# Kernel tuning notes

Measured on AMD Instinct MI355X. Metric: run time of the kernel, lower is better.

The kernel has to match this reference:

```python
import jax, jax.numpy as jnp
import numpy as np

L, D, H, F = 2, 512, 8, 2048
B, S = 1, 2048
DH = D // H
EPS = 1e-6
NEG = -1e9


def setup_inputs() -> dict:
    key = jax.random.key(0)
    ks = jax.random.split(key, 8)
    s = 0.02
    return {
        "x": jax.random.normal(ks[0], (B, S, D), jnp.float32),
        "enc_output": jax.random.normal(ks[1], (B, S, D), jnp.float32),
        # per-layer stacked params; axis 1 of attn weights = [wq, wk, wv, wo]
        "attn1_w": jax.random.normal(ks[2], (L, 4, D, D), jnp.float32) * s,
        "attn1_b": jnp.zeros((L, 4, D), jnp.float32),
        "attn2_w": jax.random.normal(ks[3], (L, 4, D, D), jnp.float32) * s,
        "attn2_b": jnp.zeros((L, 4, D), jnp.float32),
        "ffn_w1": jax.random.normal(ks[4], (L, D, F), jnp.float32) * s,
        "ffn_b1": jnp.zeros((L, F), jnp.float32),
        "ffn_w2": jax.random.normal(ks[5], (L, F, D), jnp.float32) * s,
        "ffn_b2": jnp.zeros((L, D), jnp.float32),
        # axis 1 = [norm1, norm2, norm3]
        "ln_g": jnp.ones((L, 3, D), jnp.float32),
        "ln_b": jnp.zeros((L, 3, D), jnp.float32),
    }


def positional_encoding(seq_len, num_feat):
    pos = jnp.arange(seq_len, dtype=jnp.float32)[:, None]
    dims = jnp.arange(num_feat, dtype=jnp.float32)[None, :]
    rates = 1.0 / jnp.power(10000.0, 2.0 * jnp.floor(dims / 2.0) / num_feat)
    ang = pos * rates  # [S, D]
    # keras module concatenates sines(even cols) and cosines(odd cols)
    return jnp.concatenate([jnp.sin(ang[:, 0::2]), jnp.cos(ang[:, 1::2])], axis=-1)[None]


def layer_norm(x, g, b):
    mu = jnp.mean(x, axis=-1, keepdims=True)
    var = jnp.mean(jnp.square(x - mu), axis=-1, keepdims=True)
    return (x - mu) * jax.lax.rsqrt(var + EPS) * g + b


def split_heads(x):
    b, s, _ = x.shape
    return x.reshape(b, s, H, DH).transpose(0, 2, 1, 3)  # [B,H,S,dh]


def mha(q_in, k_in, v_in, w, bias, mask):
    q = split_heads(q_in @ w[0] + bias[0])
    k = split_heads(k_in @ w[1] + bias[1])
    v = split_heads(v_in @ w[2] + bias[2])
    logits = jnp.einsum("bhqd,bhkd->bhqk", q, k) / jnp.sqrt(jnp.float32(DH))
    if mask is not None:
        logits = logits + mask * NEG
    weights = jax.nn.softmax(logits, axis=-1)
    out = jnp.einsum("bhqk,bhkd->bhqd", weights, v)
    b, _, s, _ = out.shape
    out = out.transpose(0, 2, 1, 3).reshape(b, s, D)
    return out @ w[3] + bias[3]


def decoder_forward(x, enc_output, attn1_w, attn1_b, attn2_w, attn2_b,
                    ffn_w1, ffn_b1, ffn_w2, ffn_b2, ln_g, ln_b):
    s = x.shape[1]
    x = x + positional_encoding(s, x.shape[2])
    causal = jnp.triu(jnp.ones((s, s), jnp.float32), k=1)[None, None]  # 1 = masked

    def layer(x, p):
        a1w, a1b, a2w, a2b, w1, b1, w2, b2, g, bn = p
        attn1 = mha(x, x, x, a1w, a1b, causal)
        x = layer_norm(x + attn1, g[0], bn[0])
        attn2 = mha(x, enc_output, enc_output, a2w, a2b, None)
        x = layer_norm(x + attn2, g[1], bn[1])
        ffn = jax.nn.relu(x @ w1 + b1) @ w2 + b2
        x = layer_norm(x + ffn, g[2], bn[2])
        return x, None

    x, _ = jax.lax.scan(layer, x, (attn1_w, attn1_b, attn2_w, attn2_b,
                                   ffn_w1, ffn_b1, ffn_w2, ffn_b2, ln_g, ln_b))
    return x


def reference(x, enc_output, attn1_w, attn1_b, attn2_w, attn2_b,
              ffn_w1, ffn_b1, ffn_w2, ffn_b2, ln_g, ln_b):
    return decoder_forward(x, enc_output, attn1_w, attn1_b, attn2_w, attn2_b,
                           ffn_w1, ffn_b1, ffn_w2, ffn_b2, ln_g, ln_b)
```

## Files before the change

kernel.cpp:

```cpp
#include <hip/hip_runtime.h>
#include <hip/hip_bf16.h>
#include <math.h>

#define S 2048
#define D 512
#define H 8
#define DH 64
#define F 2048
#define NLAYER 2

typedef __attribute__((ext_vector_type(8))) short bf16x8;
typedef __attribute__((ext_vector_type(4))) float f32x4;
typedef __hip_bfloat16 bf16;

typedef __attribute__((address_space(3))) unsigned int lds_u32;
typedef __attribute__((address_space(1))) const unsigned int glb_u32;

__device__ __forceinline__ void gld16(const void* g, void* l) {
    __builtin_amdgcn_global_load_lds((glb_u32*)g, (lds_u32*)l, 16, 0, 0);
}

__global__ void prep_kernel(const float* __restrict__ x, const float* __restrict__ enc,
                            float* __restrict__ xbF, bf16* __restrict__ xbB,
                            bf16* __restrict__ encB) {
    int idx = blockIdx.x * blockDim.x + threadIdx.x;
    if (idx >= S * D) return;
    int s = idx / D;
    int j = idx % D;
    int jj = (j < D / 2) ? j : j - D / 2;
    float rate = expf(-(float)jj * (logf(10000.0f) / (float)(D / 2)));
    float ang = (float)s * rate;
    float pe = (j < D / 2) ? sinf(ang) : cosf(ang);
    float v = x[idx] + pe;
    xbF[idx] = v;
    xbB[idx] = __float2bfloat16(v);
    encB[idx] = __float2bfloat16(enc[idx]);
}

__global__ __launch_bounds__(256)
void transpose_cvt_b(const float* __restrict__ in, bf16* __restrict__ out, int R, int C,
                     size_t inStride, size_t outL, size_t outM, int mpl)
{
    __shared__ float t[64][65];
    const int z = blockIdx.z;
    const float* src = in + (size_t)z * inStride;
    bf16* dst = out + (size_t)(z / mpl) * outL + (size_t)(z % mpl) * outM;
    const int rb = blockIdx.x * 64, cb = blockIdx.y * 64;
    for (int i = threadIdx.x; i < 4096; i += 256) {
        int r = i >> 6, c = i & 63;
        t[r][c] = src[(size_t)(rb + r) * C + cb + c];
    }
    __syncthreads();
    for (int i = threadIdx.x; i < 4096; i += 256) {
        int r = i >> 6, c = i & 63;
        dst[(size_t)(cb + r) * R + rb + c] = __float2bfloat16(t[c][r]);
    }
}

template<int BM, int BN, int BK, int MODE>
__global__ __launch_bounds__(256)
void gemm_bf16(const bf16* __restrict__ A, const bf16* __restrict__ Bt,
               const float* __restrict__ bias, float* __restrict__ outF,
               bf16* __restrict__ outB, int K, int ldc, int relu,
               bf16* __restrict__ q16, bf16* __restrict__ kh,
               bf16* __restrict__ vt, int qn, int kn)
{
    constexpr int MI = BM / 32, NJ = BN / 32;
    constexpr int SL = BK / 8;
    constexpr int KS = BK / 32;
    constexpr int HALF = (BM + BN) * BK * 2;
    constexpr int IA = BM * SL / 256, IB = BN * SL / 256;
    constexpr int TS = BN + 8;
    constexpr int LDS_VB = (MODE == 1) ? BM * TS * 2 : 0;
    constexpr int LDSZ = (2 * HALF > LDS_VB) ? 2 * HALF : LDS_VB;
    __shared__ char lds[LDSZ];
    const int tid = threadIdx.x;
    const int w = tid >> 6, l = tid & 63;
    const int l15 = l & 15, l4 = l >> 4;
    const int bm = blockIdx.y * BM, bn = blockIdx.x * BN;
    const int wr = (w >> 1) * (BM / 2), wc = (w & 1) * (BN / 2);

    f32x4 acc[MI][NJ] = {};

#define XV(row) ((BK == 64) ? ((row) & 7) : (((row) >> 1) & 3))
#define GSTAGE(k0, b)                                                          \
    {                                                                          \
        _Pragma("unroll")                                                      \
        for (int i = 0; i < IA; ++i) {                                         \
            int n = (w * IA + i) * 64 + l;                                     \
            int row = n / SL;                                                  \
            int sl = (n % SL) ^ XV(row);                                       \
            gld16(A + (size_t)(bm + row) * K + (k0) + sl * 8,                  \
                  lds + (b) * HALF + (w * IA + i) * 1024);                     \
        }                                                                      \
        _Pragma("unroll")                                                      \
        for (int i = 0; i < IB; ++i) {                                         \
            int n = (w * IB + i) * 64 + l;                                     \
            int row = n / SL;                                                  \
            int sl = (n % SL) ^ XV(row);                                       \
            gld16(Bt + (size_t)(bn + row) * K + (k0) + sl * 8,                 \
                  lds + (b) * HALF + BM * BK * 2 + (w * IB + i) * 1024);       \
        }                                                                      \
    }

    GSTAGE(0, 0);
    __syncthreads();
    int cur = 0;
    for (int k0 = 0; k0 < K; k0 += BK) {
        if (k0 + BK < K) GSTAGE(k0 + BK, cur ^ 1);
        const char* base = lds + cur * HALF;
        bf16x8 af[MI][KS], bfr[NJ][KS];
#pragma unroll
        for (int i = 0; i < MI; ++i) {
            int row = wr + i * 16 + l15;
#pragma unroll
            for (int s = 0; s < KS; ++s)
                af[i][s] = *(const bf16x8*)(base + row * (BK * 2)
                                            + (((s * 4 + l4) ^ XV(row)) << 4));
        }
#pragma unroll
        for (int j = 0; j < NJ; ++j) {
            int row = wc + j * 16 + l15;
#pragma unroll
            for (int s = 0; s < KS; ++s)
                bfr[j][s] = *(const bf16x8*)(base + BM * BK * 2 + row * (BK * 2)
                                             + (((s * 4 + l4) ^ XV(row)) << 4));
        }
#pragma unroll
        for (int s = 0; s < KS; ++s)
#pragma unroll
            for (int i = 0; i < MI; ++i)
#pragma unroll
                for (int j = 0; j < NJ; ++j)
                    acc[i][j] = __builtin_amdgcn_mfma_f32_16x16x32_bf16(af[i][s], bfr[j][s], acc[i][j], 0, 0, 0);
        __syncthreads();
        cur ^= 1;
    }
#undef GSTAGE
#undef XV

    if (MODE == 0) {
#pragma unroll
        for (int i = 0; i < MI; ++i)
#pragma unroll
            for (int j = 0; j < NJ; ++j)
#pragma unroll
                for (int q = 0; q < 4; ++q) {
                    int row = bm + wr + i * 16 + l4 * 4 + q;
                    int col = bn + wc + j * 16 + l15;
                    float v = acc[i][j][q] + bias[col];
                    if (relu) v = fmaxf(v, 0.f);
                    if (outF) outF[(size_t)row * ldc + col] = v;
                    if (outB) outB[(size_t)row * ldc + col] = __float2bfloat16(v);
                }
    } else {
        const int creg = (bn < qn) ? 0 : (bn < qn + kn ? 1 : 2);
        if (creg < 2) {
#pragma unroll
            for (int i = 0; i < MI; ++i)
#pragma unroll
                for (int j = 0; j < NJ; ++j)
#pragma unroll
                    for (int q = 0; q < 4; ++q) {
                        int row = bm + wr + i * 16 + l4 * 4 + q;
                        int col = bn + wc + j * 16 + l15;
                        float v = acc[i][j][q] + bias[col];
                        if (creg == 0) {
                            q16[(size_t)row * 512 + col] = __float2bfloat16(v);
                        } else {
                            int c2 = col - qn;
                            kh[((size_t)(c2 >> 6) * S + row) * 64 + (c2 & 63)] = __float2bfloat16(v);
                        }
                    }
        } else {
            short* t = (short*)lds;
#pragma unroll
            for (int i = 0; i < MI; ++i)
#pragma unroll
                for (int j = 0; j < NJ; ++j)
#pragma unroll
                    for (int q = 0; q < 4; ++q) {
                        int r = wr + i * 16 + l4 * 4 + q;
                        int c = wc + j * 16 + l15;
                        float v = acc[i][j][q] + bias[bn + c];
                        t[r * TS + c] = __builtin_bit_cast(short, __float2bfloat16(v));
                    }
            __syncthreads();
            const int dgb = bn - qn - kn;
            constexpr int SGR = BM / 8;
            for (int i2 = tid; i2 < BN * SGR; i2 += 256) {
                int dl = i2 / SGR;
                int s8 = (i2 % SGR) * 8;
                bf16x8 v;
#pragma unroll
                for (int jj = 0; jj < 8; ++jj)
                    v[jj] = t[(s8 + jj) * TS + dl];
                *(bf16x8*)(vt + (size_t)(dgb + dl) * S + bm + s8) = v;
            }
        }
    }
}

template<int CAUSAL>
__global__ __launch_bounds__(512)
void attn_mfma7(const bf16* __restrict__ Q, const bf16* __restrict__ Kh,
                const bf16* __restrict__ Vt, bf16* __restrict__ O)
{
    __shared__ char lds[82944];
    const int tid = threadIdx.x;
    const int w = tid >> 6, l = tid & 63;
    const int l15 = l & 15, l4 = l >> 4;
    const int g = w >> 2, wl = w & 3;
    const int h = blockIdx.x, qb = blockIdx.y;
    const int qw = qb * 64 + wl * 16;
    const int qr = qw + l15;
    char* plds = lds + 65536 + w * 2048;

    const float QSC = 0.1803368801f;
    bf16x8 aq[2];
#pragma unroll
    for (int s = 0; s < 2; ++s) {
        bf16x8 raw = *(const bf16x8*)(Q + (size_t)(qw + l15) * 512 + h * DH + s * 32 + l4 * 8);
#pragma unroll
        for (int j = 0; j < 8; ++j) {
            float f = __builtin_bit_cast(float, ((unsigned int)(unsigned short)raw[j]) << 16) * QSC;
            raw[j] = __builtin_bit_cast(short, __float2bfloat16(f));
        }
        aq[s] = raw;
    }

    f32x4 o[4] = {};
    float mrun = -1e30f, lrun = 0.f;
    const int cmax = CAUSAL ? qb : (S / 64 - 1);
    const int nits = cmax / 2 + 1;

#define STAGE(ii, p)                                                                \
    {                                                                               \
        const int cc = 2 * (ii) + g;                                                \
        if (cc <= cmax) {                                                           \
            const int kb2 = cc * 64;                                                \
            _Pragma("unroll")                                                       \
            for (int i = 0; i < 2; ++i) {                                           \
                int n = wl * 128 + i * 64 + l;                                      \
                int row = n >> 3;                                                   \
                int sl = (n & 7) ^ (row & 7);                                       \
                gld16(Kh + ((size_t)h * S + kb2 + row) * 64 + sl * 8,               \
                      lds + (p) * 32768 + g * 16384 + wl * 2048 + i * 1024);        \
                gld16(Vt + ((size_t)(h * 64 + row)) * S + kb2 + sl * 8,             \
                      lds + (p) * 32768 + g * 16384 + 8192 + wl * 2048 + i * 1024); \
            }                                                                       \
        }                                                                           \
    }

    STAGE(0, 0);
    __syncthreads();

    int cur = 0;
    for (int it = 0; it < nits; ++it) {
        if (it + 1 < nits) STAGE(it + 1, cur ^ 1);
        const int c = 2 * it + g;
        if (c <= cmax) {
            const char* kb = lds + cur * 32768 + g * 16384;
            const char* vb = kb + 8192;
            const int kbase = c * 64;

            f32x4 st[4];
            __builtin_amdgcn_s_setprio(1);
#pragma unroll
            for (int t = 0; t < 4; ++t) {
                f32x4 sacc = {0.f, 0.f, 0.f, 0.f};
#pragma unroll
                for (int s = 0; s < 2; ++s) {
                    bf16x8 kf = *(const bf16x8*)(kb + (t * 16 + l15) * 128
                                                 + (((s * 4 + l4) ^ (l15 & 7)) << 4));
                    sacc = __builtin_amdgcn_mfma_f32_16x16x32_bf16(kf, aq[s], sacc, 0, 0, 0);
                }
                st[t] = sacc;
            }
            __builtin_amdgcn_s_setprio(0);

            float mx = -1e30f;
#pragma unroll
            for (int t = 0; t < 4; ++t)
#pragma unroll
                for (int r = 0; r < 4; ++r) {
                    float v = st[t][r];
                    if (CAUSAL && c == cmax) {
                        int key = kbase + t * 16 + l4 * 4 + r;
                        if (key > qr) v = -1e30f;
                    }
                    st[t][r] = v;
                    mx = fmaxf(mx, v);
                }
            mx = fmaxf(mx, __shfl_xor(mx, 16));
            mx = fmaxf(mx, __shfl_xor(mx, 32));

            if (__any(mx > mrun + 8.0f)) {
                float mnew = fmaxf(mrun, mx);
                float scl = exp2f(mrun - mnew);
                mrun = mnew;
                lrun *= scl;
#pragma unroll
                for (int j = 0; j < 4; ++j) {
                    float sj = __shfl(scl, (l & 48) | (l4 * 4 + j));
#pragma unroll
                    for (int dt = 0; dt < 4; ++dt) o[dt][j] *= sj;
                }
            }

            float ps = 0.f;
#pragma unroll
            for (int t = 0; t < 4; ++t) {
                float e0 = exp2f(st[t][0] - mrun);
                float e1 = exp2f(st[t][1] - mrun);
                float e2 = exp2f(st[t][2] - mrun);
                float e3 = exp2f(st[t][3] - mrun);
                ps += (e0 + e1) + (e2 + e3);
                unsigned int lo = (unsigned int)(unsigned short)__builtin_bit_cast(short, __float2bfloat16(e0))
                                | ((unsigned int)(unsigned short)__builtin_bit_cast(short, __float2bfloat16(e1)) << 16);
                unsigned int hi = (unsigned int)(unsigned short)__builtin_bit_cast(short, __float2bfloat16(e2))
                                | ((unsigned int)(unsigned short)__builtin_bit_cast(short, __float2bfloat16(e3)) << 16);
                uint2 pk; pk.x = lo; pk.y = hi;
                int byte = (l15 * 128 + t * 32 + l4 * 8) ^ ((l15 & 7) << 4);
                *(uint2*)(plds + byte) = pk;
            }
            ps += __shfl_xor(ps, 16);
            ps += __shfl_xor(ps, 32);
            lrun += ps;

            bf16x8 pf[2];
#pragma unroll
            for (int s = 0; s < 2; ++s) {
                int byte = (l15 * 128 + s * 64 + l4 * 16) ^ ((l15 & 7) << 4);
                pf[s] = *(const bf16x8*)(plds + byte);
            }
            __builtin_amdgcn_s_setprio(1);
#pragma unroll
            for (int dt = 0; dt < 4; ++dt)
#pragma unroll
                for (int s = 0; s < 2; ++s) {
                    bf16x8 vf = *(const bf16x8*)(vb + (dt * 16 + l15) * 128
                                                 + (((s * 4 + l4) ^ (l15 & 7)) << 4));
                    o[dt] = __builtin_amdgcn_mfma_f32_16x16x32_bf16(pf[s], vf, o[dt], 0, 0, 0);
                }
            __builtin_amdgcn_s_setprio(0);
        }
        __syncthreads();
        cur ^= 1;
    }
#undef STAGE

#pragma unroll
    for (int dt = 0; dt < 4; ++dt)
#pragma unroll
        for (int j = 0; j < 4; ++j) {
            int q = l4 * 4 + j;
            int d = dt * 16 + l15;
            int byte = q * 128 + ((d * 2) ^ ((q & 7) << 4));
            *(short*)(plds + byte) = __builtin_bit_cast(short, __float2bfloat16(o[dt][j]));
        }
    if (l < 16) {
        *(float*)(lds + 81920 + w * 128 + l * 8) = mrun;
        *(float*)(lds + 81920 + w * 128 + l * 8 + 4) = lrun;
    }
    __syncthreads();

    {
        const int qt16 = tid >> 7;
        const int idx = tid & 127;
        const int q = idx >> 3;
        const int d0 = (idx & 7) * 8;
        const char* p0 = lds + 65536 + qt16 * 2048;
        const char* p1 = lds + 65536 + (qt16 + 4) * 2048;
        float m0 = *(const float*)(lds + 81920 + qt16 * 128 + q * 8);
        float l0 = *(const float*)(lds + 81920 + qt16 * 128 + q * 8 + 4);
        float m1 = *(const float*)(lds + 81920 + (qt16 + 4) * 128 + q * 8);
        float l1 = *(const float*)(lds + 81920 + (qt16 + 4) * 128 + q * 8 + 4);
        float mt = fmaxf(m0, m1);
        float f0 = exp2f(m0 - mt), f1 = exp2f(m1 - mt);
        float lt = f0 * l0 + f1 * l1;
        float inv = 1.f / lt;
        int byte = q * 128 + ((d0 * 2) ^ ((q & 7) << 4));
        bf16x8 a = *(const bf16x8*)(p0 + byte);
        bf16x8 b = *(const bf16x8*)(p1 + byte);
        bf16x8 r;
#pragma unroll
        for (int jj = 0; jj < 8; ++jj) {
            float va = __builtin_bit_cast(float, ((unsigned int)(unsigned short)a[jj]) << 16);
            float vb2 = __builtin_bit_cast(float, ((unsigned int)(unsigned short)b[jj]) << 16);
            r[jj] = __builtin_bit_cast(short, __float2bfloat16((f0 * va + f1 * vb2) * inv));
        }
        *(bf16x8*)(O + (size_t)(qb * 64 + qt16 * 16 + q) * D + h * DH + d0) = r;
    }
}

__global__ __launch_bounds__(128)
void add_ln_kernel(const float* __restrict__ a, const float* __restrict__ b,
                   const float* __restrict__ g, const float* __restrict__ beta,
                   float* __restrict__ outF, bf16* __restrict__ outB)
{
    const int row = blockIdx.x;
    const int tid = threadIdx.x;
    float4 av = *(const float4*)&a[(size_t)row * D + tid * 4];
    float4 bv = *(const float4*)&b[(size_t)row * D + tid * 4];
    float4 s;
    s.x = av.x + bv.x; s.y = av.y + bv.y; s.z = av.z + bv.z; s.w = av.w + bv.w;
    float sum = s.x + s.y + s.z + s.w;
    float sq = s.x * s.x + s.y * s.y + s.z * s.z + s.w * s.w;
#pragma unroll
    for (int off = 32; off > 0; off >>= 1) {
        sum += __shfl_xor(sum, off);
        sq  += __shfl_xor(sq, off);
    }
    __shared__ float red[4];
    if ((tid & 63) == 0) { red[(tid >> 6) * 2] = sum; red[(tid >> 6) * 2 + 1] = sq; }
    __syncthreads();
    sum = red[0] + red[2];
    sq  = red[1] + red[3];
    float mu = sum / (float)D;
    float var = sq / (float)D - mu * mu;
    float rs = rsqrtf(var + 1e-6f);
    float4 gv = *(const float4*)&g[tid * 4];
    float4 bt = *(const float4*)&beta[tid * 4];
    float4 o;
    o.x = (s.x - mu) * rs * gv.x + bt.x;
    o.y = (s.y - mu) * rs * gv.y + bt.y;
    o.z = (s.z - mu) * rs * gv.z + bt.z;
    o.w = (s.w - mu) * rs * gv.w + bt.w;
    *(float4*)&outF[(size_t)row * D + tid * 4] = o;
    if (outB) {
        outB[(size_t)row * D + tid * 4 + 0] = __float2bfloat16(o.x);
        outB[(size_t)row * D + tid * 4 + 1] = __float2bfloat16(o.y);
        outB[(size_t)row * D + tid * 4 + 2] = __float2bfloat16(o.z);
        outB[(size_t)row * D + tid * 4 + 3] = __float2bfloat16(o.w);
    }
}

extern "C" void kernel_launch(void* const* d_in, const int* in_sizes, int n_in,
                              void* d_out, int out_size, void* d_ws, size_t ws_size,
                              hipStream_t stream)
{
    const float* x   = (const float*)d_in[0];
    const float* enc = (const float*)d_in[1];
    const float* a1w = (const float*)d_in[2];
    const float* a1b = (const float*)d_in[3];
    const float* a2w = (const float*)d_in[4];
    const float* a2b = (const float*)d_in[5];
    const float* fw1 = (const float*)d_in[6];
    const float* fb1 = (const float*)d_in[7];
    const float* fw2 = (const float*)d_in[8];
    const float* fb2 = (const float*)d_in[9];
    const float* lng = (const float*)d_in[10];
    const float* lnb = (const float*)d_in[11];
    float* out = (float*)d_out;

    char* wsb = (char*)d_ws;
    float* xb   = (float*)(wsb);
    float* ao   = (float*)(wsb + ((size_t)4 << 20));
    bf16* xb16  = (bf16*)(wsb + ((size_t)8 << 20));
    bf16* enc16 = (bf16*)(wsb + ((size_t)10 << 20));
    bf16* att16 = (bf16*)(wsb + ((size_t)12 << 20));
    bf16* q16   = (bf16*)(wsb + ((size_t)14 << 20));
    bf16* kh16  = (bf16*)(wsb + ((size_t)16 << 20));
    bf16* vt16  = (bf16*)(wsb + ((size_t)18 << 20));
    bf16* ffh16 = att16;
    bf16* wts   = (bf16*)(wsb + ((size_t)20 << 20));
    const size_t WCH = 1048576;
    const size_t DD = (size_t)D * D, DF = (size_t)D * F;

    transpose_cvt_b<<<dim3(8, 8, 8), 256, 0, stream>>>(a1w, wts,            D, D, DD, WCH, DD, 4);
    transpose_cvt_b<<<dim3(8, 8, 8), 256, 0, stream>>>(a2w, wts + 2 * WCH,  D, D, DD, WCH, DD, 4);
    transpose_cvt_b<<<dim3(8, 32, 2), 256, 0, stream>>>(fw1, wts + 4 * WCH, D, F, DF, WCH, 0, 1);
    transpose_cvt_b<<<dim3(32, 8, 2), 256, 0, stream>>>(fw2, wts + 6 * WCH, F, D, DF, WCH, 0, 1);
    prep_kernel<<<(S * D + 255) / 256, 256, 0, stream>>>(x, enc, xb, xb16, enc16);

    for (int l = 0; l < NLAYER; ++l) {
        const bf16* A1T = wts + (size_t)(0 + l) * WCH;
        const bf16* A2T = wts + (size_t)(2 + l) * WCH;
        const bf16* W1T = wts + (size_t)(4 + l) * WCH;
        const bf16* W2T = wts + (size_t)(6 + l) * WCH;
        const float* b1v = a1b + (size_t)l * 4 * D;
        const float* b2v = a2b + (size_t)l * 4 * D;

        gemm_bf16<64, 64, 64, 1><<<dim3(24, 32), 256, 0, stream>>>(
            xb16, A1T, b1v, nullptr, nullptr, D, 0, 0, q16, kh16, vt16, 512, 512);
        attn_mfma7<1><<<dim3(H, S / 64), 512, 0, stream>>>(q16, kh16, vt16, att16);
        gemm_bf16<32, 64, 64, 0><<<dim3(8, 64), 256, 0, stream>>>(
            att16, A1T + 3 * DD, b1v + 3 * D, ao, nullptr, D, D, 0, nullptr, nullptr, nullptr, 0, 0);
        add_ln_kernel<<<S, 128, 0, stream>>>(xb, ao, lng + (size_t)(l * 3 + 0) * D, lnb + (size_t)(l * 3 + 0) * D, xb, xb16);

        gemm_bf16<32, 64, 64, 0><<<dim3(8, 64), 256, 0, stream>>>(
            xb16, A2T, b2v, nullptr, q16, D, 512, 0, nullptr, nullptr, nullptr, 0, 0);
        gemm_bf16<64, 64, 64, 1><<<dim3(16, 32), 256, 0, stream>>>(
            enc16, A2T + DD, b2v + D, nullptr, nullptr, D, 0, 0, q16, kh16, vt16, 0, 512);
        attn_mfma7<0><<<dim3(H, S / 64), 512, 0, stream>>>(q16, kh16, vt16, att16);
        gemm_bf16<32, 64, 64, 0><<<dim3(8, 64), 256, 0, stream>>>(
            att16, A2T + 3 * DD, b2v + 3 * D, ao, nullptr, D, D, 0, nullptr, nullptr, nullptr, 0, 0);
        add_ln_kernel<<<S, 128, 0, stream>>>(xb, ao, lng + (size_t)(l * 3 + 1) * D, lnb + (size_t)(l * 3 + 1) * D, xb, xb16);

        gemm_bf16<64, 64, 64, 0><<<dim3(32, 32), 256, 0, stream>>>(
            xb16, W1T, fb1 + (size_t)l * F, nullptr, ffh16, D, F, 1, nullptr, nullptr, nullptr, 0, 0);
        gemm_bf16<32, 64, 64, 0><<<dim3(8, 64), 256, 0, stream>>>(
            ffh16, W2T, fb2 + (size_t)l * D, ao, nullptr, F, D, 0, nullptr, nullptr, nullptr, 0, 0);
        float* dstF = (l == NLAYER - 1) ? out : xb;
        bf16* dstB = (l == NLAYER - 1) ? nullptr : xb16;
        add_ln_kernel<<<S, 128, 0, stream>>>(xb, ao, lng + (size_t)(l * 3 + 2) * D, lnb + (size_t)(l * 3 + 2) * D, dstF, dstB);
    }
}
```

Measured before the change: 289.6 us.

## Process two key chunks per wave group per stage in attention kernel

Each wave group now handles two 64-key chunks per iteration, with separate running max, sum and accumulator states that are merged at the end. The pipeline stage grows to 128 keys per group, so LDS use rises to about 145 KB and there are half as many barrier-separated iterations. Doubling in-flight MFMA work per wave is meant to give more instruction-level parallelism and cut synchronization overhead. The cost is more registers and LDS, which lowers occupancy, and the causal kernel gets coarser load balance at short rows.

```diff
diff --git a/kernel.cpp b/kernel.cpp
--- a/kernel.cpp
+++ b/kernel.cpp
@@ -203,10 +203,10 @@
 
 template<int CAUSAL>
 __global__ __launch_bounds__(512)
-void attn_mfma7(const bf16* __restrict__ Q, const bf16* __restrict__ Kh,
+void attn_mfma8(const bf16* __restrict__ Q, const bf16* __restrict__ Kh,
                 const bf16* __restrict__ Vt, bf16* __restrict__ O)
 {
-    __shared__ char lds[82944];
+    __shared__ char lds[148480];
     const int tid = threadIdx.x;
     const int w = tid >> 6, l = tid & 63;
     const int l15 = l & 15, l4 = l >> 4;
@@ -214,7 +214,7 @@
     const int h = blockIdx.x, qb = blockIdx.y;
     const int qw = qb * 64 + wl * 16;
     const int qr = qw + l15;
-    char* plds = lds + 65536 + w * 2048;
+    char* plds = lds + 131072 + w * 2048;
 
     const float QSC = 0.1803368801f;
     bf16x8 aq[2];
@@ -229,25 +229,27 @@
         aq[s] = raw;
     }
 
-    f32x4 o[4] = {};
-    float mrun = -1e30f, lrun = 0.f;
+    f32x4 oA[4] = {}, oB[4] = {};
+    float mA = -1e30f, lA = 0.f, mB = -1e30f, lB = 0.f;
     const int cmax = CAUSAL ? qb : (S / 64 - 1);
-    const int nits = cmax / 2 + 1;
+    const int nits = cmax / 4 + 1;
 
 #define STAGE(ii, p)                                                                \
     {                                                                               \
-        const int cc = 2 * (ii) + g;                                                \
-        if (cc <= cmax) {                                                           \
-            const int kb2 = cc * 64;                                                \
+        const int c0s = 4 * (ii) + 2 * g;                                           \
+        if (c0s <= cmax) {                                                          \
+            const int kb2 = c0s * 64;                                               \
             _Pragma("unroll")                                                       \
-            for (int i = 0; i < 2; ++i) {                                           \
-                int n = wl * 128 + i * 64 + l;                                      \
-                int row = n >> 3;                                                   \
-                int sl = (n & 7) ^ (row & 7);                                       \
-                gld16(Kh + ((size_t)h * S + kb2 + row) * 64 + sl * 8,               \
-                      lds + (p) * 32768 + g * 16384 + wl * 2048 + i * 1024);        \
-                gld16(Vt + ((size_t)(h * 64 + row)) * S + kb2 + sl * 8,             \
-                      lds + (p) * 32768 + g * 16384 + 8192 + wl * 2048 + i * 1024); \
+            for (int i = 0; i < 4; ++i) {                                           \
+                int n = wl * 256 + i * 64 + l;                                      \
+                int rowk = n >> 3;                                                  \
+                int slk = (n & 7) ^ (rowk & 7);                                     \
+                gld16(Kh + ((size_t)h * S + kb2 + rowk) * 64 + slk * 8,             \
+                      lds + (p) * 65536 + g * 32768 + wl * 4096 + i * 1024);        \
+                int rowv = n >> 4;                                                  \
+                int slv = (n & 15) ^ (rowv & 7);                                    \
+                gld16(Vt + ((size_t)(h * 64 + rowv)) * S + kb2 + slv * 8,           \
+                      lds + (p) * 65536 + g * 32768 + 16384 + wl * 4096 + i * 1024);\
             }                                                                       \
         }                                                                           \
     }
@@ -258,14 +260,15 @@
     int cur = 0;
     for (int it = 0; it < nits; ++it) {
         if (it + 1 < nits) STAGE(it + 1, cur ^ 1);
-        const int c = 2 * it + g;
-        if (c <= cmax) {
-            const char* kb = lds + cur * 32768 + g * 16384;
-            const char* vb = kb + 8192;
-            const int kbase = c * 64;
-
-            f32x4 st[4];
-            __builtin_amdgcn_s_setprio(1);
+        const int c0 = 4 * it + 2 * g;
+        const char* kb = lds + cur * 65536 + g * 32768;
+        const char* vb = kb + 16384;
+        const int actA = (c0 <= cmax);
+        const int actB = (c0 + 1 <= cmax);
+
+        f32x4 stA[4], stB[4];
+        __builtin_amdgcn_s_setprio(1);
+        if (actA) {
 #pragma unroll
             for (int t = 0; t < 4; ++t) {
                 f32x4 sacc = {0.f, 0.f, 0.f, 0.f};
@@ -275,80 +278,108 @@
                                                  + (((s * 4 + l4) ^ (l15 & 7)) << 4));
                     sacc = __builtin_amdgcn_mfma_f32_16x16x32_bf16(kf, aq[s], sacc, 0, 0, 0);
                 }
-                st[t] = sacc;
+                stA[t] = sacc;
             }
-            __builtin_amdgcn_s_setprio(0);
-
-            float mx = -1e30f;
-#pragma unroll
-            for (int t = 0; t < 4; ++t)
-#pragma unroll
-                for (int r = 0; r < 4; ++r) {
-                    float v = st[t][r];
-                    if (CAUSAL && c == cmax) {
-                        int key = kbase + t * 16 + l4 * 4 + r;
-                        if (key > qr) v = -1e30f;
-                    }
-                    st[t][r] = v;
-                    mx = fmaxf(mx, v);
+        }
+        if (actB) {
+#pragma unroll
+            for (int t = 0; t < 4; ++t) {
+                f32x4 sacc = {0.f, 0.f, 0.f, 0.f};
+#pragma unroll
+                for (int s = 0; s < 2; ++s) {
+                    bf16x8 kf = *(const bf16x8*)(kb + (64 + t * 16 + l15) * 128
+                                                 + (((s * 4 + l4) ^ (l15 & 7)) << 4));
+                    sacc = __builtin_amdgcn_mfma_f32_16x16x32_bf16(kf, aq[s], sacc, 0, 0, 0);
                 }
-            mx = fmaxf(mx, __shfl_xor(mx, 16));
-            mx = fmaxf(mx, __shfl_xor(mx, 32));
-
-            if (__any(mx > mrun + 8.0f)) {
-                float mnew = fmaxf(mrun, mx);
-                float scl = exp2f(mrun - mnew);
-                mrun = mnew;
-                lrun *= scl;
-#pragma unroll
-                for (int j = 0; j < 4; ++j) {
-                    float sj = __shfl(scl, (l & 48) | (l4 * 4 + j));
-#pragma unroll
-                    for (int dt = 0; dt < 4; ++dt) o[dt][j] *= sj;
-                }
+                stB[t] = sacc;
             }
-
-            float ps = 0.f;
-#pragma unroll
-            for (int t = 0; t < 4; ++t) {
-                float e0 = exp2f(st[t][0] - mrun);
-                float e1 = exp2f(st[t][1] - mrun);
-                float e2 = exp2f(st[t][2] - mrun);
-                float e3 = exp2f(st[t][3] - mrun);
-                ps += (e0 + e1) + (e2 + e3);
-                unsigned int lo = (unsigned int)(unsigned short)__builtin_bit_cast(short, __float2bfloat16(e0))
-                                | ((unsigned int)(unsigned short)__builtin_bit_cast(short, __float2bfloat16(e1)) << 16);
-                unsigned int hi = (unsigned int)(unsigned short)__builtin_bit_cast(short, __float2bfloat16(e2))
-                                | ((unsigned int)(unsigned short)__builtin_bit_cast(short, __float2bfloat16(e3)) << 16);
-                uint2 pk; pk.x = lo; pk.y = hi;
-                int byte = (l15 * 128 + t * 32 + l4 * 8) ^ ((l15 & 7) << 4);
-                *(uint2*)(plds + byte) = pk;
-            }
-            ps += __shfl_xor(ps, 16);
-            ps += __shfl_xor(ps, 32);
-            lrun += ps;
-
-            bf16x8 pf[2];
-#pragma unroll
-            for (int s = 0; s < 2; ++s) {
-                int byte = (l15 * 128 + s * 64 + l4 * 16) ^ ((l15 & 7) << 4);
-                pf[s] = *(const bf16x8*)(plds + byte);
-            }
-            __builtin_amdgcn_s_setprio(1);
-#pragma unroll
-            for (int dt = 0; dt < 4; ++dt)
-#pragma unroll
-                for (int s = 0; s < 2; ++s) {
-                    bf16x8 vf = *(const bf16x8*)(vb + (dt * 16 + l15) * 128
-                                                 + (((s * 4 + l4) ^ (l15 & 7)) << 4));
-                    o[dt] = __builtin_amdgcn_mfma_f32_16x16x32_bf16(pf[s], vf, o[dt], 0, 0, 0);
-                }
-            __builtin_amdgcn_s_setprio(0);
-        }
+        }
+        __builtin_amdgcn_s_setprio(0);
+
+#define SOFTMAX(st, mrun, lrun, o, cc)                                              \
+        {                                                                           \
+            float mx = -1e30f;                                                      \
+            _Pragma("unroll")                                                       \
+            for (int t = 0; t < 4; ++t)                                             \
+                _Pragma("unroll")                                                   \
+                for (int r = 0; r < 4; ++r) {                                       \
+                    float v = st[t][r];                                             \
+                    if (CAUSAL && (cc) == cmax) {                                   \
+                        int key = (cc) * 64 + t * 16 + l4 * 4 + r;                  \
+                        if (key > qr) v = -1e30f;                                   \
+                    }                                                               \
+                    st[t][r] = v;                                                   \
+                    mx = fmaxf(mx, v);                                              \
+                }                                                                   \
+            mx = fmaxf(mx, __shfl_xor(mx, 16));                                     \
+            mx = fmaxf(mx, __shfl_xor(mx, 32));                                     \
+            if (__any(mx > mrun + 8.0f)) {                                          \
+                float mnew = fmaxf(mrun, mx);                                       \
+                float scl = exp2f(mrun - mnew);                                     \
+                mrun = mnew;                                                        \
+                lrun *= scl;                                                        \
+                _Pragma("unroll")                                                   \
+                for (int j = 0; j < 4; ++j) {                                       \
+                    float sj = __shfl(scl, (l & 48) | (l4 * 4 + j));                \
+                    _Pragma("unroll")                                               \
+                    for (int dt = 0; dt < 4; ++dt) o[dt][j] *= sj;                  \
+                }                                                                   \
+            }                                                                       \
+        }
+        if (actA) SOFTMAX(stA, mA, lA, oA, c0);
+        if (actB) SOFTMAX(stB, mB, lB, oB, c0 + 1);
+#undef SOFTMAX
+
+#define PPV(st, mrun, lrun, o, jch)                                                 \
+        {                                                                           \
+            float ps = 0.f;                                                         \
+            _Pragma("unroll")                                                       \
+            for (int t = 0; t < 4; ++t) {                                           \
+                float e0 = exp2f(st[t][0] - mrun);                                  \
+                float e1 = exp2f(st[t][1] - mrun);                                  \
+                float e2 = exp2f(st[t][2] - mrun);                                  \
+                float e3 = exp2f(st[t][3] - mrun);                                  \
+                ps += (e0 + e1) + (e2 + e3);                                        \
+                unsigned int lo = (unsigned int)(unsigned short)__builtin_bit_cast(short, __float2bfloat16(e0))  \
+                                | ((unsigned int)(unsigned short)__builtin_bit_cast(short, __float2bfloat16(e1)) << 16); \
+                unsigned int hi = (unsigned int)(unsigned short)__builtin_bit_cast(short, __float2bfloat16(e2))  \
+                                | ((unsigned int)(unsigned short)__builtin_bit_cast(short, __float2bfloat16(e3)) << 16); \
+                uint2 pk; pk.x = lo; pk.y = hi;                                     \
+                int byte = (l15 * 128 + t * 32 + l4 * 8) ^ ((l15 & 7) << 4);        \
+                *(uint2*)(plds + byte) = pk;                                        \
+            }                                                                       \
+            ps += __shfl_xor(ps, 16);                                               \
+            ps += __shfl_xor(ps, 32);                                               \
+            lrun += ps;                                                             \
+            bf16x8 pf[2];                                                           \
+            _Pragma("unroll")                                                       \
+            for (int s = 0; s < 2; ++s) {                                           \
+                int byte = (l15 * 128 + s * 64 + l4 * 16) ^ ((l15 & 7) << 4);       \
+                pf[s] = *(const bf16x8*)(plds + byte);                              \
+            }                                                                       \
+            __builtin_amdgcn_s_setprio(1);                                          \
+            _Pragma("unroll")                                                       \
+            for (int dt = 0; dt < 4; ++dt)                                          \
+                _Pragma("unroll")                                                   \
+                for (int s = 0; s < 2; ++s) {                                       \
+                    bf16x8 vf = *(const bf16x8*)(vb + (dt * 16 + l15) * 256         \
+                                 + ((((jch) * 8 + s * 4 + l4) ^ (l15 & 7)) << 4));  \
+                    o[dt] = __builtin_amdgcn_mfma_f32_16x16x32_bf16(pf[s], vf, o[dt], 0, 0, 0); \
+                }                                                                   \
+            __builtin_amdgcn_s_setprio(0);                                          \
+        }
+        if (actA) PPV(stA, mA, lA, oA, 0);
+        if (actB) PPV(stB, mB, lB, oB, 1);
+#undef PPV
+
         __syncthreads();
         cur ^= 1;
     }
 #undef STAGE
+
+    float mw = fmaxf(mA, mB);
+    float fA = exp2f(mA - mw), fB = exp2f(mB - mw);
+    float lw = fA * lA + fB * lB;
 
 #pragma unroll
     for (int dt = 0; dt < 4; ++dt)
@@ -356,12 +387,13 @@
         for (int j = 0; j < 4; ++j) {
             int q = l4 * 4 + j;
             int d = dt * 16 + l15;
+            float ov = fA * oA[dt][j] + fB * oB[dt][j];
             int byte = q * 128 + ((d * 2) ^ ((q & 7) << 4));
-            *(short*)(plds + byte) = __builtin_bit_cast(short, __float2bfloat16(o[dt][j]));
+            *(short*)(plds + byte) = __builtin_bit_cast(short, __float2bfloat16(ov));
         }
     if (l < 16) {
-        *(float*)(lds + 81920 + w * 128 + l * 8) = mrun;
-        *(float*)(lds + 81920 + w * 128 + l * 8 + 4) = lrun;
+        *(float*)(lds + 147456 + w * 128 + l * 8) = mw;
+        *(float*)(lds + 147456 + w * 128 + l * 8 + 4) = lw;
     }
     __syncthreads();
 
@@ -370,12 +402,12 @@
         const int idx = tid & 127;
         const int q = idx >> 3;
         const int d0 = (idx & 7) * 8;
-        const char* p0 = lds + 65536 + qt16 * 2048;
-        const char* p1 = lds + 65536 + (qt16 + 4) * 2048;
-        float m0 = *(const float*)(lds + 81920 + qt16 * 128 + q * 8);
-        float l0 = *(const float*)(lds + 81920 + qt16 * 128 + q * 8 + 4);
-        float m1 = *(const float*)(lds + 81920 + (qt16 + 4) * 128 + q * 8);
-        float l1 = *(const float*)(lds + 81920 + (qt16 + 4) * 128 + q * 8 + 4);
+        const char* p0 = lds + 131072 + qt16 * 2048;
+        const char* p1 = lds + 131072 + (qt16 + 4) * 2048;
+        float m0 = *(const float*)(lds + 147456 + qt16 * 128 + q * 8);
+        float l0 = *(const float*)(lds + 147456 + qt16 * 128 + q * 8 + 4);
+        float m1 = *(const float*)(lds + 147456 + (qt16 + 4) * 128 + q * 8);
+        float l1 = *(const float*)(lds + 147456 + (qt16 + 4) * 128 + q * 8 + 4);
         float mt = fmaxf(m0, m1);
         float f0 = exp2f(m0 - mt), f1 = exp2f(m1 - mt);
         float lt = f0 * l0 + f1 * l1;
@@ -484,7 +516,7 @@
 
         gemm_bf16<64, 64, 64, 1><<<dim3(24, 32), 256, 0, stream>>>(
             xb16, A1T, b1v, nullptr, nullptr, D, 0, 0, q16, kh16, vt16, 512, 512);
-        attn_mfma7<1><<<dim3(H, S / 64), 512, 0, stream>>>(q16, kh16, vt16, att16);
+        attn_mfma8<1><<<dim3(H, S / 64), 512, 0, stream>>>(q16, kh16, vt16, att16);
         gemm_bf16<32, 64, 64, 0><<<dim3(8, 64), 256, 0, stream>>>(
             att16, A1T + 3 * DD, b1v + 3 * D, ao, nullptr, D, D, 0, nullptr, nullptr, nullptr, 0, 0);
         add_ln_kernel<<<S, 128, 0, stream>>>(xb, ao, lng + (size_t)(l * 3 + 0) * D, lnb + (size_t)(l * 3 + 0) * D, xb, xb16);
@@ -493,7 +525,7 @@
             xb16, A2T, b2v, nullptr, q16, D, 512, 0, nullptr, nullptr, nullptr, 0, 0);
         gemm_bf16<64, 64, 64, 1><<<dim3(16, 32), 256, 0, stream>>>(
             enc16, A2T + DD, b2v + D, nullptr, nullptr, D, 0, 0, q16, kh16, vt16, 0, 512);
-        attn_mfma7<0><<<dim3(H, S / 64), 512, 0, stream>>>(q16, kh16, vt16, att16);
+        attn_mfma8<0><<<dim3(H, S / 64), 512, 0, stream>>>(q16, kh16, vt16, att16);
         gemm_bf16<32, 64, 64, 0><<<dim3(8, 64), 256, 0, stream>>>(
             att16, A2T + 3 * DD, b2v + 3 * D, ao, nullptr, D, D, 0, nullptr, nullptr, nullptr, 0, 0);
         add_ln_kernel<<<S, 128, 0, stream>>>(xb, ao, lng + (size_t)(l * 3 + 1) * D, lnb + (size_t)(l * 3 + 1) * D, xb, xb16);
```

New measurement: 296.0 us. 2.2% more time.
